# Kernel optimization log

Measured on AMD Instinct MI355X. Metric: run time of the kernel, lower is better.

## Reference

```python
import jax, jax.numpy as jnp
import numpy as np

B, S, D = 4, 2048, 1024
H = 16
HD = D // H  # 64


def setup_inputs() -> dict:
    key = jax.random.key(0)
    ks = jax.random.split(key, 6)
    scale = 1.0 / np.sqrt(D)
    return {
        "x": jax.random.normal(ks[0], (B, S, D), dtype=jnp.float32),
        "W_q": jax.random.normal(ks[1], (D, D), dtype=jnp.float32) * scale,
        "W_k": jax.random.normal(ks[2], (D, D), dtype=jnp.float32) * scale,
        "W_v": jax.random.normal(ks[3], (D, D), dtype=jnp.float32) * scale,
        "W_o": jax.random.normal(ks[4], (D, D), dtype=jnp.float32) * scale,
        "b_o": jax.random.normal(ks[5], (D,), dtype=jnp.float32) * 0.01,
    }


def reference(x, W_q, W_k, W_v, W_o, b_o):
    b, n, _ = x.shape
    # projections (Linear stores weight as [out,in]; here W_* are [in,out])
    q = (x @ W_q).reshape(b, n, H, HD).transpose(0, 2, 1, 3)  # [b,h,n,hd]
    k = (x @ W_k).reshape(b, n, H, HD).transpose(0, 2, 1, 3)
    v = (x @ W_v).reshape(b, n, H, HD).transpose(0, 2, 1, 3)
    scores = jnp.einsum("bhqd,bhkd->bhqk", q, k) / np.sqrt(HD).astype(np.float32)
    causal = jnp.tril(jnp.ones((n, n), dtype=bool))  # True = keep
    scores = jnp.where(causal, scores, -jnp.inf)
    weights = jax.nn.softmax(scores, axis=-1)
    ctx = jnp.einsum("bhqk,bhkd->bhqd", weights, v)
    ctx = ctx.transpose(0, 2, 1, 3).reshape(b, n, D)
    return ctx @ W_o + b_o
```

## Files before the change

### kernel.cpp

```cpp
#include <hip/hip_runtime.h>
#include <cstdint>

#define S_LEN 2048
#define D_MODEL 1024
#define NH 16
#define HDIM 64
#define BATCH 4

typedef __attribute__((ext_vector_type(8))) __bf16 bfrag;
typedef __attribute__((ext_vector_type(4))) float ffrag;

__device__ __forceinline__ unsigned short f2bf(float f) {
    union { float f; uint32_t u; } v; v.f = f;
    uint32_t u = v.u;
    u += 0x7fff + ((u >> 16) & 1);
    return (unsigned short)(u >> 16);
}

__device__ __forceinline__ bfrag ld_frag(const unsigned short* p) {
    union { uint4 u; bfrag b; } x;
    x.u = *(const uint4*)p;
    return x.b;
}

__device__ __forceinline__ float fast_exp2(float x) {
#if __has_builtin(__builtin_amdgcn_exp2f)
    return __builtin_amdgcn_exp2f(x);
#else
    return __expf(x * 0.6931471805599453f);
#endif
}

__device__ __forceinline__ uint32_t pack_bf16(float a, float b) {
    union { float f; uint32_t u; } x, y; x.f = a; y.f = b;
    return __builtin_amdgcn_perm(y.u + 0x8000u, x.u + 0x8000u, 0x07060302u);
}

__device__ __forceinline__ void g2l16(const unsigned short* g, unsigned short* l) {
    __builtin_amdgcn_global_load_lds(
        (const __attribute__((address_space(1))) void*)g,
        (__attribute__((address_space(3))) void*)l, 16, 0, 0);
}

__global__ __launch_bounds__(256) void prep_kernel(const float* __restrict__ x,
                                                   const float* __restrict__ w0,
                                                   const float* __restrict__ w1,
                                                   const float* __restrict__ w2,
                                                   const float* __restrict__ w3,
                                                   unsigned short* __restrict__ xb,
                                                   unsigned short* __restrict__ wt) {
    __shared__ float tile[32][33];
    int bid = blockIdx.x;
    int t = threadIdx.x;
    if (bid < 4096) {
        int i = bid * 256 + t;
        const float4* p = (const float4*)x + (size_t)i * 2;
        float4 a = p[0], b = p[1];
        union { unsigned short u[8]; uint4 v; } o;
        o.u[0]=f2bf(a.x); o.u[1]=f2bf(a.y); o.u[2]=f2bf(a.z); o.u[3]=f2bf(a.w);
        o.u[4]=f2bf(b.x); o.u[5]=f2bf(b.y); o.u[6]=f2bf(b.z); o.u[7]=f2bf(b.w);
        ((uint4*)xb)[i] = o.v;
    } else {
        int r = bid - 4096;
        int mat = r >> 10;
        int rem = r & 1023;
        const float* w = (mat == 0) ? w0 : (mat == 1) ? w1 : (mat == 2) ? w2 : w3;
        int n0 = (rem & 31) * 32, k0 = (rem >> 5) * 32;
        int tx = t & 31, ty = t >> 5;
        for (int i = 0; i < 32; i += 8)
            tile[ty + i][tx] = w[(size_t)(k0 + ty + i) * D_MODEL + n0 + tx];
        __syncthreads();
        unsigned short* o = wt + (size_t)mat * D_MODEL * D_MODEL;
        for (int i = 0; i < 32; i += 8)
            o[(size_t)(n0 + ty + i) * D_MODEL + (k0 + tx)] = f2bf(tile[tx][ty + i]);
    }
}

__global__ __launch_bounds__(256) void transpose_v_kernel(const unsigned short* __restrict__ Vb,
                                                          unsigned short* __restrict__ Vtb) {
    __shared__ unsigned short tile[64][72];
    int st = blockIdx.x;
    int bh = blockIdx.y;
    int t = threadIdx.x;
    int sl = t >> 2, dc = (t & 3) * 16;
    const unsigned short* src = Vb + ((size_t)bh * S_LEN + st * 64 + sl) * HDIM + dc;
    *(uint4*)&tile[sl][dc]     = *(const uint4*)(src);
    *(uint4*)&tile[sl][dc + 8] = *(const uint4*)(src + 8);
    __syncthreads();
    int d = t >> 2, sc = (t & 3) * 16;
    union { unsigned short u[16]; uint4 v[2]; } o;
#pragma unroll
    for (int i = 0; i < 16; i++) o.u[i] = tile[sc + i][d];
    unsigned short* dst = Vtb + ((size_t)bh * HDIM + d) * S_LEN + st * 64 + sc;
    *(uint4*)(dst)     = o.v[0];
    *(uint4*)(dst + 8) = o.v[1];
}

#define GBUF 4096

__global__ __launch_bounds__(256) void gemm_kernel(
    const unsigned short* __restrict__ A,
    const unsigned short* __restrict__ Bt,
    int mode,
    unsigned short* __restrict__ Qb,
    unsigned short* __restrict__ Kb,
    unsigned short* __restrict__ Vb,
    float* __restrict__ Out,
    const float* __restrict__ bias) {
    __shared__ unsigned short As[2 * GBUF];
    __shared__ unsigned short Bs[2 * GBUF];
    int t = threadIdx.x;
    int m0 = blockIdx.y * 128;
    int n0 = blockIdx.x * 128;
    int wave = t >> 6, lane = t & 63;
    int quad = lane >> 4, lrow = lane & 15;
    int wm = (wave & 1) * 64, wn = (wave >> 1) * 64;

    ffrag acc[4][4];
    const ffrag fz = {0.f, 0.f, 0.f, 0.f};
    for (int i = 0; i < 4; i++)
        for (int j = 0; j < 4; j++) acc[i][j] = fz;

    int c0 = t, c1 = 256 + t;
    int r0 = c0 >> 2, cg0 = (c0 & 3) ^ ((r0 >> 1) & 3);
    int r1 = c1 >> 2, cg1 = (c1 & 3) ^ ((r1 >> 1) & 3);
    const unsigned short* A0 = A + (size_t)(m0 + r0) * D_MODEL + cg0 * 8;
    const unsigned short* A1 = A + (size_t)(m0 + r1) * D_MODEL + cg1 * 8;
    const unsigned short* B0 = Bt + (size_t)(n0 + r0) * D_MODEL + cg0 * 8;
    const unsigned short* B1 = Bt + (size_t)(n0 + r1) * D_MODEL + cg1 * 8;
    unsigned short* lA0 = &As[(wave * 64) * 8];
    unsigned short* lA1 = &As[(256 + wave * 64) * 8];
    unsigned short* lB0 = &Bs[(wave * 64) * 8];
    unsigned short* lB1 = &Bs[(256 + wave * 64) * 8];

    g2l16(A0, lA0);
    g2l16(A1, lA1);
    g2l16(B0, lB0);
    g2l16(B1, lB1);

    for (int k0 = 0; k0 < D_MODEL; k0 += 32) {
        int buf = ((k0 >> 5) & 1) * GBUF;
        __syncthreads();
        if (k0 + 32 < D_MODEL) {
            int nb = (((k0 >> 5) + 1) & 1) * GBUF;
            g2l16(A0 + k0 + 32, lA0 + nb);
            g2l16(A1 + k0 + 32, lA1 + nb);
            g2l16(B0 + k0 + 32, lB0 + nb);
            g2l16(B1 + k0 + 32, lB1 + nb);
        }
        bfrag af[4], bf[4];
        for (int mi = 0; mi < 4; mi++) {
            int row = wm + mi * 16 + lrow;
            af[mi] = ld_frag(&As[buf + row * 32 + ((quad ^ ((row >> 1) & 3)) * 8)]);
        }
        for (int ni = 0; ni < 4; ni++) {
            int row = wn + ni * 16 + lrow;
            bf[ni] = ld_frag(&Bs[buf + row * 32 + ((quad ^ ((row >> 1) & 3)) * 8)]);
        }
        for (int mi = 0; mi < 4; mi++)
            for (int ni = 0; ni < 4; ni++)
                acc[mi][ni] = __builtin_amdgcn_mfma_f32_16x16x32_bf16(af[mi], bf[ni], acc[mi][ni], 0, 0, 0);
    }

    for (int mi = 0; mi < 4; mi++) {
        int row = m0 + wm + mi * 16 + quad * 4;
        for (int ni = 0; ni < 4; ni++) {
            int col = n0 + wn + ni * 16 + lrow;
            for (int r = 0; r < 4; r++) {
                float v = acc[mi][ni][r];
                int m = row + r;
                if (mode == 0) {
                    int matid = col >> 10;
                    int nn = col & 1023;
                    int h = nn >> 6, d = nn & 63;
                    int b = m >> 11, s = m & 2047;
                    size_t bh = (size_t)(b * NH + h);
                    if (matid == 0)      Qb[(bh * S_LEN + s) * HDIM + d] = f2bf(v);
                    else if (matid == 1) Kb[(bh * S_LEN + s) * HDIM + d] = f2bf(v);
                    else                 Vb[(bh * S_LEN + s) * HDIM + d] = f2bf(v);
                } else {
                    Out[(size_t)m * D_MODEL + col] = v + bias[col];
                }
            }
        }
    }
}

#define SCALE2 0.18033688f
#define CSHIFT 4.0f
#define KVBUF 4096

__global__ __launch_bounds__(256, 4) void attn_kernel(
    const unsigned short* __restrict__ Qb,
    const unsigned short* __restrict__ Kb,
    const unsigned short* __restrict__ Vtb,
    unsigned short* __restrict__ ctxb) {
    __shared__ unsigned short Ks[2 * KVBUF];
    __shared__ unsigned short Vs[2 * KVBUF];
    __shared__ unsigned short Ps[4 * 32 * 64];
    int bx = blockIdx.x;
    int bh = blockIdx.y;
    int t = threadIdx.x;
    int wave = t >> 6, lane = t & 63;
    int quad = lane >> 4, lrow = lane & 15;
    int swz = lrow & 7;
    int ca = (quad ^ swz) * 8;
    int cb = ca ^ 32;

    union { uint4 u; bfrag b; } one_u;
    one_u.u.x = 0x3F803F80u; one_u.u.y = 0x3F803F80u;
    one_u.u.z = 0x3F803F80u; one_u.u.w = 0x3F803F80u;
    bfrag onef = one_u.b;

    const unsigned short* Qg = Qb + (size_t)bh * S_LEN * HDIM;
    const unsigned short* Kg = Kb + (size_t)bh * S_LEN * HDIM;
    const unsigned short* Vg = Vtb + (size_t)bh * HDIM * S_LEN;
    int b = bh >> 4, h = bh & 15;

    int c0 = t, c1 = 256 + t;
    int kr0 = c0 >> 3, kp0 = (c0 & 7) ^ (kr0 & 7);
    int kr1 = c1 >> 3, kp1 = (c1 & 7) ^ (kr1 & 7);
    const unsigned short* pK0 = Kg + (size_t)kr0 * HDIM + kp0 * 8;
    const unsigned short* pK1 = Kg + (size_t)kr1 * HDIM + kp1 * 8;
    const unsigned short* pV0 = Vg + (size_t)kr0 * S_LEN + kp0 * 8;
    const unsigned short* pV1 = Vg + (size_t)kr1 * S_LEN + kp1 * 8;
    unsigned short* lK0 = &Ks[(wave * 64) * 8];
    unsigned short* lK1 = &Ks[(256 + wave * 64) * 8];
    unsigned short* lV0 = &Vs[(wave * 64) * 8];
    unsigned short* lV1 = &Vs[(256 + wave * 64) * 8];
    unsigned short* Pw = &Ps[wave * 32 * 64];

    for (int ph = 0; ph < 2; ph++) {
        int qbi = ph == 0 ? (15 - bx) : bx;
        int qw = qbi * 128 + wave * 32;
        int qw_u = __builtin_amdgcn_readfirstlane(qw);
        int nk = 2 * qbi + 2;

        bfrag qf[2][2];
#pragma unroll
        for (int g = 0; g < 2; g++)
#pragma unroll
            for (int c = 0; c < 2; c++)
                qf[g][c] = ld_frag(Qg + (size_t)(qw + g * 16 + lrow) * HDIM + c * 32 + quad * 8);

        ffrag acc[2][4];
        ffrag acc_l[2];
        const ffrag fz = {0.f, 0.f, 0.f, 0.f};
#pragma unroll
        for (int g = 0; g < 2; g++) {
#pragma unroll
            for (int d = 0; d < 4; d++) acc[g][d] = fz;
            acc_l[g] = fz;
        }

        __syncthreads();
        g2l16(pK0, lK0);
        g2l16(pK1, lK1);
        g2l16(pV0, lV0);
        g2l16(pV1, lV1);

        for (int kt = 0; kt < nk; kt++) {
            int kbase = kt * 64;
            int buf = (kt & 1) * KVBUF;
            __syncthreads();
            if (kt + 1 < nk) {
                int nb = ((kt + 1) & 1) * KVBUF;
                size_t krow_off = (size_t)(kbase + 64) * HDIM;
                g2l16(pK0 + krow_off, lK0 + nb);
                g2l16(pK1 + krow_off, lK1 + nb);
                g2l16(pV0 + kbase + 64, lV0 + nb);
                g2l16(pV1 + kbase + 64, lV1 + nb);
            }

            if (kbase > qw_u + 31) continue;

#pragma unroll
            for (int g = 0; g < 2; g++) {
                if (kbase > qw_u + g * 16 + 15) continue;
                ffrag sf[4];
#pragma unroll
                for (int ki = 0; ki < 4; ki++) {
                    int krow = buf + (ki * 16 + lrow) * 64;
                    bfrag ka = ld_frag(&Ks[krow + ca]);
                    bfrag kb = ld_frag(&Ks[krow + cb]);
                    ffrag s = fz;
                    s = __builtin_amdgcn_mfma_f32_16x16x32_bf16(ka, qf[g][0], s, 0, 0, 0);
                    s = __builtin_amdgcn_mfma_f32_16x16x32_bf16(kb, qf[g][1], s, 0, 0, 0);
                    sf[ki] = s;
                }

                int qg = qw + g * 16 + lrow;
                bool need_mask = (kbase + 63) > (qw_u + g * 16);
                float sv[16];
#pragma unroll
                for (int ki = 0; ki < 4; ki++)
#pragma unroll
                    for (int r = 0; r < 4; r++) {
                        float v = sf[ki][r];
                        if (need_mask) {
                            int key = kbase + ki * 16 + quad * 4 + r;
                            v = (key <= qg) ? v : -3.0e38f;
                        }
                        sv[ki * 4 + r] = fast_exp2(__builtin_fmaf(v, SCALE2, -CSHIFT));
                    }
                int prow = (g * 16 + lrow) * 64;
#pragma unroll
                for (int ki = 0; ki < 4; ki++) {
                    uint2 w2;
                    w2.x = pack_bf16(sv[ki * 4 + 0], sv[ki * 4 + 1]);
                    w2.y = pack_bf16(sv[ki * 4 + 2], sv[ki * 4 + 3]);
                    int pc = ((ki * 2 + (quad >> 1)) ^ swz) * 8 + (quad & 1) * 4;
                    *(uint2*)&Pw[prow + pc] = w2;
                }
            }

            bfrag pf[2][2];
#pragma unroll
            for (int g = 0; g < 2; g++) {
                if (kbase > qw_u + g * 16 + 15) continue;
                int prow = (g * 16 + lrow) * 64;
                pf[g][0] = ld_frag(&Pw[prow + ca]);
                pf[g][1] = ld_frag(&Pw[prow + cb]);
                acc_l[g] = __builtin_amdgcn_mfma_f32_16x16x32_bf16(onef, pf[g][0], acc_l[g], 0, 0, 0);
                acc_l[g] = __builtin_amdgcn_mfma_f32_16x16x32_bf16(onef, pf[g][1], acc_l[g], 0, 0, 0);
            }
#pragma unroll
            for (int di = 0; di < 4; di++) {
                int vrow = buf + (di * 16 + lrow) * 64;
                bfrag va = ld_frag(&Vs[vrow + ca]);
                bfrag vb = ld_frag(&Vs[vrow + cb]);
#pragma unroll
                for (int g = 0; g < 2; g++) {
                    if (kbase > qw_u + g * 16 + 15) continue;
                    acc[g][di] = __builtin_amdgcn_mfma_f32_16x16x32_bf16(va, pf[g][0], acc[g][di], 0, 0, 0);
                    acc[g][di] = __builtin_amdgcn_mfma_f32_16x16x32_bf16(vb, pf[g][1], acc[g][di], 0, 0, 0);
                }
            }
        }

#pragma unroll
        for (int g = 0; g < 2; g++) {
            float rl = __builtin_amdgcn_rcpf(acc_l[g][0]);
#pragma unroll
            for (int di = 0; di < 4; di++) {
                uint2 w2;
                w2.x = pack_bf16(acc[g][di][0] * rl, acc[g][di][1] * rl);
                w2.y = pack_bf16(acc[g][di][2] * rl, acc[g][di][3] * rl);
                *(uint2*)&Pw[lrow * 72 + di * 16 + quad * 4] = w2;
            }
            int ql = lane >> 3, cc = lane & 7;
#pragma unroll
            for (int p = 0; p < 2; p++) {
                uint4 vv = *(uint4*)&Pw[(p * 8 + ql) * 72 + cc * 8];
                int q = qw + g * 16 + p * 8 + ql;
                *(uint4*)(ctxb + ((size_t)b * S_LEN + q) * D_MODEL + h * HDIM + cc * 8) = vv;
            }
        }
    }
}

extern "C" void kernel_launch(void* const* d_in, const int* in_sizes, int n_in,
                              void* d_out, int out_size, void* d_ws, size_t ws_size,
                              hipStream_t stream) {
    const float* x   = (const float*)d_in[0];
    const float* W_q = (const float*)d_in[1];
    const float* W_k = (const float*)d_in[2];
    const float* W_v = (const float*)d_in[3];
    const float* W_o = (const float*)d_in[4];
    const float* b_o = (const float*)d_in[5];
    float* out = (float*)d_out;

    unsigned short* xb   = (unsigned short*)d_ws;
    unsigned short* Wt   = xb + (size_t)8192 * 1024;
    unsigned short* Qb   = Wt + (size_t)4 * 1024 * 1024;
    unsigned short* Kb   = Qb + (size_t)64 * 2048 * 64;
    unsigned short* Vtb  = Kb + (size_t)64 * 2048 * 64;
    unsigned short* ctxb = Vtb + (size_t)64 * 2048 * 64;
    unsigned short* Vb   = ctxb;
    unsigned short* Wto  = Wt + (size_t)3 * 1024 * 1024;

    prep_kernel<<<8192, 256, 0, stream>>>(x, W_q, W_k, W_v, W_o, xb, Wt);
    gemm_kernel<<<dim3(24, 64), 256, 0, stream>>>(xb, Wt, 0, Qb, Kb, Vb, nullptr, nullptr);
    transpose_v_kernel<<<dim3(32, 64), 256, 0, stream>>>(Vb, Vtb);
    attn_kernel<<<dim3(8, 64), 256, 0, stream>>>(Qb, Kb, Vtb, ctxb);
    gemm_kernel<<<dim3(8, 64), 256, 0, stream>>>(ctxb, Wto, 1, nullptr, nullptr, nullptr, out, b_o);
}
```

Baseline: 294.8 us.

## Shrink attention query tile to 64 rows per block and double grid

The attention kernel now gives each block 64 query rows (16 per wave) instead of 128 (32 per wave), with paired causal chunks (31-bx, bx) and a grid of 16x64 blocks. Per-wave work drops to one 16-row group, which removes the per-group skip branches and halves register and P-tile shared memory use. This raises block count and occupancy and simplifies masking to the last key tile. The cost is that each K/V tile loaded into shared memory is now reused by half as many query rows, so global-to-LDS traffic roughly doubles.

```diff
diff --git a/kernel.cpp b/kernel.cpp
--- a/kernel.cpp
+++ b/kernel.cpp
@@ -197,7 +197,7 @@
     unsigned short* __restrict__ ctxb) {
     __shared__ unsigned short Ks[2 * KVBUF];
     __shared__ unsigned short Vs[2 * KVBUF];
-    __shared__ unsigned short Ps[4 * 32 * 64];
+    __shared__ unsigned short Ps[4 * 16 * 64];
     int bx = blockIdx.x;
     int bh = blockIdx.y;
     int t = threadIdx.x;
@@ -228,30 +228,24 @@
     unsigned short* lK1 = &Ks[(256 + wave * 64) * 8];
     unsigned short* lV0 = &Vs[(wave * 64) * 8];
     unsigned short* lV1 = &Vs[(256 + wave * 64) * 8];
-    unsigned short* Pw = &Ps[wave * 32 * 64];
+    unsigned short* Pw = &Ps[wave * 16 * 64];
 
     for (int ph = 0; ph < 2; ph++) {
-        int qbi = ph == 0 ? (15 - bx) : bx;
-        int qw = qbi * 128 + wave * 32;
-        int qw_u = __builtin_amdgcn_readfirstlane(qw);
-        int nk = 2 * qbi + 2;
-
-        bfrag qf[2][2];
-#pragma unroll
-        for (int g = 0; g < 2; g++)
-#pragma unroll
-            for (int c = 0; c < 2; c++)
-                qf[g][c] = ld_frag(Qg + (size_t)(qw + g * 16 + lrow) * HDIM + c * 32 + quad * 8);
-
-        ffrag acc[2][4];
-        ffrag acc_l[2];
+        int qc = ph == 0 ? (31 - bx) : bx;
+        int qw = qc * 64 + wave * 16;
+        int nk = qc + 1;
+
+        bfrag qf[2];
+#pragma unroll
+        for (int c = 0; c < 2; c++)
+            qf[c] = ld_frag(Qg + (size_t)(qw + lrow) * HDIM + c * 32 + quad * 8);
+
+        ffrag acc[4];
+        ffrag acc_l;
         const ffrag fz = {0.f, 0.f, 0.f, 0.f};
 #pragma unroll
-        for (int g = 0; g < 2; g++) {
-#pragma unroll
-            for (int d = 0; d < 4; d++) acc[g][d] = fz;
-            acc_l[g] = fz;
-        }
+        for (int d = 0; d < 4; d++) acc[d] = fz;
+        acc_l = fz;
 
         __syncthreads();
         g2l16(pK0, lK0);
@@ -272,89 +266,70 @@
                 g2l16(pV1 + kbase + 64, lV1 + nb);
             }
 
-            if (kbase > qw_u + 31) continue;
-
-#pragma unroll
-            for (int g = 0; g < 2; g++) {
-                if (kbase > qw_u + g * 16 + 15) continue;
-                ffrag sf[4];
-#pragma unroll
-                for (int ki = 0; ki < 4; ki++) {
-                    int krow = buf + (ki * 16 + lrow) * 64;
-                    bfrag ka = ld_frag(&Ks[krow + ca]);
-                    bfrag kb = ld_frag(&Ks[krow + cb]);
-                    ffrag s = fz;
-                    s = __builtin_amdgcn_mfma_f32_16x16x32_bf16(ka, qf[g][0], s, 0, 0, 0);
-                    s = __builtin_amdgcn_mfma_f32_16x16x32_bf16(kb, qf[g][1], s, 0, 0, 0);
-                    sf[ki] = s;
+            ffrag sf[4];
+#pragma unroll
+            for (int ki = 0; ki < 4; ki++) {
+                int krow = buf + (ki * 16 + lrow) * 64;
+                bfrag ka = ld_frag(&Ks[krow + ca]);
+                bfrag kb = ld_frag(&Ks[krow + cb]);
+                ffrag s = fz;
+                s = __builtin_amdgcn_mfma_f32_16x16x32_bf16(ka, qf[0], s, 0, 0, 0);
+                s = __builtin_amdgcn_mfma_f32_16x16x32_bf16(kb, qf[1], s, 0, 0, 0);
+                sf[ki] = s;
+            }
+
+            int qg = qw + lrow;
+            bool need_mask = (kt == nk - 1);
+            float sv[16];
+#pragma unroll
+            for (int ki = 0; ki < 4; ki++)
+#pragma unroll
+                for (int r = 0; r < 4; r++) {
+                    float v = sf[ki][r];
+                    if (need_mask) {
+                        int key = kbase + ki * 16 + quad * 4 + r;
+                        v = (key <= qg) ? v : -3.0e38f;
+                    }
+                    sv[ki * 4 + r] = fast_exp2(__builtin_fmaf(v, SCALE2, -CSHIFT));
                 }
-
-                int qg = qw + g * 16 + lrow;
-                bool need_mask = (kbase + 63) > (qw_u + g * 16);
-                float sv[16];
-#pragma unroll
-                for (int ki = 0; ki < 4; ki++)
-#pragma unroll
-                    for (int r = 0; r < 4; r++) {
-                        float v = sf[ki][r];
-                        if (need_mask) {
-                            int key = kbase + ki * 16 + quad * 4 + r;
-                            v = (key <= qg) ? v : -3.0e38f;
-                        }
-                        sv[ki * 4 + r] = fast_exp2(__builtin_fmaf(v, SCALE2, -CSHIFT));
-                    }
-                int prow = (g * 16 + lrow) * 64;
-#pragma unroll
-                for (int ki = 0; ki < 4; ki++) {
-                    uint2 w2;
-                    w2.x = pack_bf16(sv[ki * 4 + 0], sv[ki * 4 + 1]);
-                    w2.y = pack_bf16(sv[ki * 4 + 2], sv[ki * 4 + 3]);
-                    int pc = ((ki * 2 + (quad >> 1)) ^ swz) * 8 + (quad & 1) * 4;
-                    *(uint2*)&Pw[prow + pc] = w2;
-                }
-            }
-
-            bfrag pf[2][2];
-#pragma unroll
-            for (int g = 0; g < 2; g++) {
-                if (kbase > qw_u + g * 16 + 15) continue;
-                int prow = (g * 16 + lrow) * 64;
-                pf[g][0] = ld_frag(&Pw[prow + ca]);
-                pf[g][1] = ld_frag(&Pw[prow + cb]);
-                acc_l[g] = __builtin_amdgcn_mfma_f32_16x16x32_bf16(onef, pf[g][0], acc_l[g], 0, 0, 0);
-                acc_l[g] = __builtin_amdgcn_mfma_f32_16x16x32_bf16(onef, pf[g][1], acc_l[g], 0, 0, 0);
-            }
+            int prow = lrow * 64;
+#pragma unroll
+            for (int ki = 0; ki < 4; ki++) {
+                uint2 w2;
+                w2.x = pack_bf16(sv[ki * 4 + 0], sv[ki * 4 + 1]);
+                w2.y = pack_bf16(sv[ki * 4 + 2], sv[ki * 4 + 3]);
+                int pc = ((ki * 2 + (quad >> 1)) ^ swz) * 8 + (quad & 1) * 4;
+                *(uint2*)&Pw[prow + pc] = w2;
+            }
+
+            bfrag pf0 = ld_frag(&Pw[prow + ca]);
+            bfrag pf1 = ld_frag(&Pw[prow + cb]);
+            acc_l = __builtin_amdgcn_mfma_f32_16x16x32_bf16(onef, pf0, acc_l, 0, 0, 0);
+            acc_l = __builtin_amdgcn_mfma_f32_16x16x32_bf16(onef, pf1, acc_l, 0, 0, 0);
 #pragma unroll
             for (int di = 0; di < 4; di++) {
                 int vrow = buf + (di * 16 + lrow) * 64;
                 bfrag va = ld_frag(&Vs[vrow + ca]);
                 bfrag vb = ld_frag(&Vs[vrow + cb]);
-#pragma unroll
-                for (int g = 0; g < 2; g++) {
-                    if (kbase > qw_u + g * 16 + 15) continue;
-                    acc[g][di] = __builtin_amdgcn_mfma_f32_16x16x32_bf16(va, pf[g][0], acc[g][di], 0, 0, 0);
-                    acc[g][di] = __builtin_amdgcn_mfma_f32_16x16x32_bf16(vb, pf[g][1], acc[g][di], 0, 0, 0);
-                }
-            }
-        }
-
-#pragma unroll
-        for (int g = 0; g < 2; g++) {
-            float rl = __builtin_amdgcn_rcpf(acc_l[g][0]);
-#pragma unroll
-            for (int di = 0; di < 4; di++) {
-                uint2 w2;
-                w2.x = pack_bf16(acc[g][di][0] * rl, acc[g][di][1] * rl);
-                w2.y = pack_bf16(acc[g][di][2] * rl, acc[g][di][3] * rl);
-                *(uint2*)&Pw[lrow * 72 + di * 16 + quad * 4] = w2;
-            }
-            int ql = lane >> 3, cc = lane & 7;
-#pragma unroll
-            for (int p = 0; p < 2; p++) {
-                uint4 vv = *(uint4*)&Pw[(p * 8 + ql) * 72 + cc * 8];
-                int q = qw + g * 16 + p * 8 + ql;
-                *(uint4*)(ctxb + ((size_t)b * S_LEN + q) * D_MODEL + h * HDIM + cc * 8) = vv;
-            }
+                acc[di] = __builtin_amdgcn_mfma_f32_16x16x32_bf16(va, pf0, acc[di], 0, 0, 0);
+                acc[di] = __builtin_amdgcn_mfma_f32_16x16x32_bf16(vb, pf1, acc[di], 0, 0, 0);
+            }
+        }
+
+        float rl = __builtin_amdgcn_rcpf(acc_l[0]);
+#pragma unroll
+        for (int di = 0; di < 4; di++) {
+            uint2 w2;
+            w2.x = pack_bf16(acc[di][0] * rl, acc[di][1] * rl);
+            w2.y = pack_bf16(acc[di][2] * rl, acc[di][3] * rl);
+            *(uint2*)&Pw[lrow * 64 + di * 16 + quad * 4] = w2;
+        }
+        int ql = lane >> 3, cc = lane & 7;
+#pragma unroll
+        for (int p = 0; p < 2; p++) {
+            uint4 vv = *(uint4*)&Pw[(p * 8 + ql) * 64 + cc * 8];
+            int q = qw + p * 8 + ql;
+            *(uint4*)(ctxb + ((size_t)b * S_LEN + q) * D_MODEL + h * HDIM + cc * 8) = vv;
         }
     }
 }
@@ -382,6 +357,6 @@
     prep_kernel<<<8192, 256, 0, stream>>>(x, W_q, W_k, W_v, W_o, xb, Wt);
     gemm_kernel<<<dim3(24, 64), 256, 0, stream>>>(xb, Wt, 0, Qb, Kb, Vb, nullptr, nullptr);
     transpose_v_kernel<<<dim3(32, 64), 256, 0, stream>>>(Vb, Vtb);
-    attn_kernel<<<dim3(8, 64), 256, 0, stream>>>(Qb, Kb, Vtb, ctxb);
+    attn_kernel<<<dim3(16, 64), 256, 0, stream>>>(Qb, Kb, Vtb, ctxb);
     gemm_kernel<<<dim3(8, 64), 256, 0, stream>>>(ctxb, Wto, 1, nullptr, nullptr, nullptr, out, b_o);
 }
```

Result: faster. 288.0 us (-2.3%).
